# Kernel tuning notes

Measured on AMD Instinct MI355X. Metric: run time of the kernel, lower is better.

## Reference

```python
import jax, jax.numpy as jnp
import numpy as np

B, S, D, N, H = 2, 1024, 1024, 16, 64
R = 2 * S          # max relative length
EPS = 1e-9
INF = 1000000.0
SHIFT = 1          # q_len == context_len branch


def _forward(query, key, value, r, cls_mask, Wq, Wk, bk, Wv, bv, Wo, bo,
             r_w_bias, r_r_bias, r_kernel, r_s_bias, seg_embed, ln_gamma, ln_beta,
             token_type_mat, attention_mask):
    scale = 1.0 / np.sqrt(H).astype(np.float32)
    q = (query @ Wq).reshape(B, S, N, H) * scale          # [b,s,n,h]
    k = (key @ Wk + bk).reshape(B, S, N, H)
    v = (value @ Wv + bv).reshape(B, S, N, H)

    # content score
    content = jnp.einsum('binh,bjnh->bnij', q + r_w_bias * scale, k)

    # relative positional score with shift-gather trick
    r_head = jnp.einsum('td,dnh->tnh', r, r_kernel)        # [2S,n,h]
    pos = jnp.einsum('binh,tnh->bnit', q + r_r_bias * scale, r_head)  # [b,n,s,2S]
    pos = pos.reshape(B, N, R, S)[:, :, SHIFT:, :].reshape(B, N, S, R - SHIFT)[..., :S]
    pos = pos * cls_mask

    # token-type (segment) score: seg_embed[0]=diff, seg_embed[1]=same
    tt_bias = jnp.einsum('binh,snh->bnis', q + r_s_bias * scale, seg_embed)  # [b,n,s,2]
    diff, same = tt_bias[..., :1], tt_bias[..., 1:]
    tt = jnp.where(token_type_mat[:, None], same, diff) * cls_mask           # [b,n,s,s]

    mask = attention_mask.astype(jnp.float32)[:, None, None]                 # [b,1,1,s]
    attn_score = content + pos + tt - INF * (1.0 - mask)
    attn_prob = jax.nn.softmax(attn_score, axis=-1)

    attn_vec = jnp.einsum('bnij,bjnh->binh', attn_prob, v).reshape(B, S, N * H)
    attn_out = attn_vec @ Wo + bo

    x = query + attn_out
    mu = jnp.mean(x, axis=-1, keepdims=True)
    var = jnp.mean(jnp.square(x - mu), axis=-1, keepdims=True)
    return (x - mu) * jax.lax.rsqrt(var + EPS) * ln_gamma + ln_beta


def setup_inputs() -> dict:
    rng = jax.random.key(0)
    ks = jax.random.split(rng, 16)
    init = 0.02
    inp = {
        'query': jax.random.normal(ks[0], (B, S, D), jnp.float32),
        'key':   jax.random.normal(ks[1], (B, S, D), jnp.float32),
        'value': jax.random.normal(ks[2], (B, S, D), jnp.float32),
        'r':     jax.random.normal(ks[3], (R, D), jnp.float32),
        'cls_mask': jnp.ones((S, S), jnp.float32),
        'Wq': jax.random.normal(ks[4], (D, N * H), jnp.float32) * init,
        'Wk': jax.random.normal(ks[5], (D, N * H), jnp.float32) * init,
        'bk': jnp.zeros((N * H,), jnp.float32),
        'Wv': jax.random.normal(ks[6], (D, N * H), jnp.float32) * init,
        'bv': jnp.zeros((N * H,), jnp.float32),
        'Wo': jax.random.normal(ks[7], (N * H, D), jnp.float32) * init,
        'bo': jnp.zeros((D,), jnp.float32),
        'r_w_bias': jax.random.normal(ks[8], (N, H), jnp.float32) * init,
        'r_r_bias': jax.random.normal(ks[9], (N, H), jnp.float32) * init,
        'r_kernel': jax.random.normal(ks[10], (D, N, H), jnp.float32) * init,
        'r_s_bias': jax.random.normal(ks[11], (N, H), jnp.float32) * init,
        'seg_embed': jax.random.normal(ks[12], (2, N, H), jnp.float32) * init,
        'ln_gamma': jnp.ones((D,), jnp.float32),
        'ln_beta': jnp.zeros((D,), jnp.float32),
        'token_type_mat': jax.random.randint(ks[13], (B, S, S), 0, 2).astype(bool),
        'attention_mask': jax.random.randint(ks[14], (B, S), 0, 2).astype(jnp.int32),
    }
    return inp


def reference(query, key, value, r, cls_mask, Wq, Wk, bk, Wv, bv, Wo, bo,
              r_w_bias, r_r_bias, r_kernel, r_s_bias, seg_embed, ln_gamma, ln_beta,
              token_type_mat, attention_mask):
    return _forward(query, key, value, r, cls_mask, Wq, Wk, bk, Wv, bv, Wo, bo,
                    r_w_bias, r_r_bias, r_kernel, r_s_bias, seg_embed, ln_gamma, ln_beta,
                    token_type_mat, attention_mask)
```

## Files before the change

kernel.cpp:

```cpp
#include <hip/hip_runtime.h>

#define S_ 1024

typedef short short8 __attribute__((ext_vector_type(8)));
typedef float floatx4 __attribute__((ext_vector_type(4)));

static __device__ __forceinline__ float b2f(ushort u) {
    union { float f; unsigned int i; } x; x.i = ((unsigned int)u) << 16; return x.f;
}
static __device__ __forceinline__ ushort f2b(float f) {
    union { float f; unsigned int i; } x; x.f = f;
    unsigned int r = (x.i + 0x7fffu + ((x.i >> 16) & 1u)) >> 16;
    return (ushort)r;
}
static __device__ __forceinline__ void async_copy16(ushort* lds, const ushort* g) {
    __builtin_amdgcn_global_load_lds((const __attribute__((address_space(1))) void*)g,
                                     (__attribute__((address_space(3))) void*)lds, 16, 0, 0);
}

struct PreArgs {
    const float* csrc[4]; ushort* cdst[4];
    const float* tsrc[5]; ushort* tdst[5];
    const int* ttm; unsigned long long* ttb;
    const int* am;  unsigned long long* amb;
};
__global__ __launch_bounds__(256) void pre_kernel(PreArgs a) {
    int z = blockIdx.z, tid = threadIdx.x;
    if (z < 4) {
        const float* s = a.csrc[z];
        ushort* d = a.cdst[z];
        size_t idx = ((size_t)blockIdx.x * 256 + tid) * 8;
        float4 f0 = *(const float4*)&s[idx];
        float4 f1 = *(const float4*)&s[idx + 4];
        alignas(16) ushort u[8] = {f2b(f0.x), f2b(f0.y), f2b(f0.z), f2b(f0.w),
                                   f2b(f1.x), f2b(f1.y), f2b(f1.z), f2b(f1.w)};
        *(uint4*)&d[idx] = *(uint4*)u;
    } else if (z < 9) {
        const float* src = a.tsrc[z - 4];
        ushort* dst = a.tdst[z - 4];
        __shared__ float tile[32][33];
        int bx = (blockIdx.x & 31) * 32, by = (blockIdx.x >> 5) * 32;
        int tx = tid & 31, ty = tid >> 5;
#pragma unroll
        for (int i = 0; i < 32; i += 8)
            tile[ty + i][tx] = src[(size_t)(by + ty + i) * 1024 + bx + tx];
        __syncthreads();
#pragma unroll
        for (int i = 0; i < 32; i += 8)
            dst[(size_t)(bx + ty + i) * 1024 + by + tx] = f2b(tile[tx][ty + i]);
    } else {
        int w = tid >> 6, lane = tid & 63;
        int waveid = blockIdx.x * 4 + w;
#pragma unroll
        for (int t = 0; t < 8; t++) {
            int word = waveid * 8 + t;
            unsigned long long m = __ballot(a.ttm[(size_t)word * 64 + lane] != 0);
            if (lane == 0) a.ttb[word] = m;
        }
        if (blockIdx.x == 0 && w == 0) {
            for (int t = 0; t < 32; t++) {
                unsigned long long m = __ballot(a.am[(size_t)t * 64 + lane] != 0);
                if (lane == 0) a.amb[t] = m;
            }
        }
    }
}

struct ProjArgs {
    const ushort* A[4];
    const ushort* BT[4];
    const float* bias[4];
    ushort* C[4];
    float scale[4];
};
__global__ __launch_bounds__(256, 2) void gemm_proj(ProjArgs args) {
    int z = blockIdx.z;
    const ushort* A = args.A[z];
    const ushort* BT = args.BT[z];
    const float* bias = args.bias[z];
    ushort* C = args.C[z];
    float scale = args.scale[z];

    __shared__ alignas(16) ushort As[128 * 64];
    __shared__ alignas(16) ushort Bs[128 * 64];
    int n0 = blockIdx.x * 128, m0 = blockIdx.y * 128;
    int tid = threadIdx.x, lane = tid & 63, w = tid >> 6;
    int wm = (w >> 1) * 64, wn = (w & 1) * 64;
    int li = lane & 15, q4 = lane >> 4;
    int lrow = lane >> 3, lu = (lane & 7) ^ lrow;
    floatx4 acc[4][4] = {};
    for (int k0 = 0; k0 < 1024; k0 += 64) {
        __syncthreads();
#pragma unroll
        for (int t = 0; t < 4; t++) {
            int c = 4 * w + t;
            const ushort* ga = &A[(size_t)(m0 + 8 * c + lrow) * 1024 + k0 + 8 * lu];
            async_copy16(&As[c * 512 + lane * 8], ga);
            const ushort* gb = &BT[(size_t)(n0 + 8 * c + lrow) * 1024 + k0 + 8 * lu];
            async_copy16(&Bs[c * 512 + lane * 8], gb);
        }
        __syncthreads();
        short8 af[2][4], bf[2][4];
#pragma unroll
        for (int kk = 0; kk < 2; kk++) {
#pragma unroll
            for (int ms = 0; ms < 4; ms++)
                af[kk][ms] = *(const short8*)&As[(wm + 16 * ms + li) * 64 +
                                                (((4 * kk + q4) ^ (li & 7)) * 8)];
#pragma unroll
            for (int ns = 0; ns < 4; ns++)
                bf[kk][ns] = *(const short8*)&Bs[(wn + 16 * ns + li) * 64 +
                                                (((4 * kk + q4) ^ (li & 7)) * 8)];
        }
#pragma unroll
        for (int kk = 0; kk < 2; kk++)
#pragma unroll
            for (int ms = 0; ms < 4; ms++)
#pragma unroll
                for (int ns = 0; ns < 4; ns++)
                    acc[ms][ns] = __builtin_amdgcn_mfma_f32_16x16x32_bf16(af[kk][ms], bf[kk][ns],
                                                                          acc[ms][ns], 0, 0, 0);
    }
#pragma unroll
    for (int ns = 0; ns < 4; ns++) {
        int col = n0 + wn + 16 * ns + li;
        float bv = bias ? bias[col] : 0.f;
#pragma unroll
        for (int ms = 0; ms < 4; ms++)
#pragma unroll
            for (int rg = 0; rg < 4; rg++) {
                int row = m0 + wm + 16 * ms + 4 * q4 + rg;
                C[(size_t)row * 1024 + col] = f2b(acc[ms][ns][rg] * scale + bv);
            }
    }
}

__global__ __launch_bounds__(256, 2) void gemm_out(const ushort* __restrict__ A,
                                                   const ushort* __restrict__ BT,
                                                   const float* __restrict__ bias,
                                                   const float* __restrict__ resid,
                                                   float* __restrict__ X) {
    __shared__ alignas(16) ushort As[64 * 64];
    __shared__ alignas(16) ushort Bs[64 * 64];
    int n0 = blockIdx.x * 64, m0 = blockIdx.y * 64;
    int tid = threadIdx.x, lane = tid & 63, w = tid >> 6;
    int wm = (w >> 1) * 32, wn = (w & 1) * 32;
    int li = lane & 15, q4 = lane >> 4;
    int lrow = lane >> 3, lu = (lane & 7) ^ lrow;
    floatx4 acc[2][2] = {};
    for (int k0 = 0; k0 < 1024; k0 += 64) {
        __syncthreads();
#pragma unroll
        for (int t = 0; t < 2; t++) {
            int c = 2 * w + t;
            const ushort* ga = &A[(size_t)(m0 + 8 * c + lrow) * 1024 + k0 + 8 * lu];
            async_copy16(&As[c * 512 + lane * 8], ga);
            const ushort* gb = &BT[(size_t)(n0 + 8 * c + lrow) * 1024 + k0 + 8 * lu];
            async_copy16(&Bs[c * 512 + lane * 8], gb);
        }
        __syncthreads();
        short8 af[2][2], bf[2][2];
#pragma unroll
        for (int kk = 0; kk < 2; kk++) {
#pragma unroll
            for (int ms = 0; ms < 2; ms++)
                af[kk][ms] = *(const short8*)&As[(wm + 16 * ms + li) * 64 +
                                                (((4 * kk + q4) ^ (li & 7)) * 8)];
#pragma unroll
            for (int ns = 0; ns < 2; ns++)
                bf[kk][ns] = *(const short8*)&Bs[(wn + 16 * ns + li) * 64 +
                                                (((4 * kk + q4) ^ (li & 7)) * 8)];
        }
#pragma unroll
        for (int kk = 0; kk < 2; kk++)
#pragma unroll
            for (int ms = 0; ms < 2; ms++)
#pragma unroll
                for (int ns = 0; ns < 2; ns++)
                    acc[ms][ns] = __builtin_amdgcn_mfma_f32_16x16x32_bf16(af[kk][ms], bf[kk][ns],
                                                                          acc[ms][ns], 0, 0, 0);
    }
#pragma unroll
    for (int ns = 0; ns < 2; ns++) {
        int col = n0 + wn + 16 * ns + li;
        float bv = bias[col];
#pragma unroll
        for (int ms = 0; ms < 2; ms++)
#pragma unroll
            for (int rg = 0; rg < 4; rg++) {
                int row = m0 + wm + 16 * ms + 4 * q4 + rg;
                X[(size_t)row * 1024 + col] = acc[ms][ns][rg] + bv + resid[(size_t)row * 1024 + col];
            }
    }
}

__global__ __launch_bounds__(256, 2) void attn_kernel(
    const ushort* __restrict__ qg, const ushort* __restrict__ kg,
    const ushort* __restrict__ vg, const ushort* __restrict__ rh,
    const float* __restrict__ rwb, const float* __restrict__ rrb,
    const float* __restrict__ rsb, const float* __restrict__ seg,
    const unsigned long long* __restrict__ ttb, const unsigned long long* __restrict__ amb,
    ushort* __restrict__ av) {
    __shared__ alignas(16) ushort kt[64][72];
    __shared__ alignas(16) ushort vt[64][72];
    __shared__ alignas(16) ushort rwin[128][72];
    __shared__ alignas(16) ushort pb[4][16][72];
    __shared__ float ttd[64], tts[64];

    int i0 = blockIdx.x * 64, n = blockIdx.y, b = blockIdx.z;
    int tid = threadIdx.x, lane = tid & 63, w = tid >> 6;
    int li = lane & 15, q4 = lane >> 4;
    const float SC = 0.125f;

    {
        int r = tid >> 2, hs = (tid & 3) * 16;
        const ushort* qp = &qg[(size_t)(b * S_ + i0 + r) * 1024 + n * 64 + hs];
        alignas(16) ushort tmp[16];
        *(uint4*)&tmp[0] = *(const uint4*)&qp[0];
        *(uint4*)&tmp[8] = *(const uint4*)&qp[8];
        float d = 0.f, s = 0.f;
#pragma unroll
        for (int e = 0; e < 16; e++) {
            float qv = b2f(tmp[e]);
            int h = n * 64 + hs + e;
            rwin[r][hs + e] = f2b(qv + rwb[h] * SC);
            rwin[64 + r][hs + e] = f2b(qv + rrb[h] * SC);
            float qs = qv + rsb[h] * SC;
            d += qs * seg[h];
            s += qs * seg[1024 + h];
        }
        d += __shfl_xor(d, 1, 64); d += __shfl_xor(d, 2, 64);
        s += __shfl_xor(s, 1, 64); s += __shfl_xor(s, 2, 64);
        if ((tid & 3) == 0) { ttd[r] = d; tts[r] = s; }
    }
    __syncthreads();

    short8 aw0 = *(const short8*)&rwin[16 * w + li][8 * q4];
    short8 aw1 = *(const short8*)&rwin[16 * w + li][32 + 8 * q4];
    short8 ar0 = *(const short8*)&rwin[64 + 16 * w + li][8 * q4];
    short8 ar1 = *(const short8*)&rwin[64 + 16 * w + li][32 + 8 * q4];
    float ttd_l[4], tts_l[4];
#pragma unroll
    for (int r = 0; r < 4; r++) { ttd_l[r] = ttd[16 * w + 4 * q4 + r]; tts_l[r] = tts[16 * w + 4 * q4 + r]; }

    floatx4 o[4] = {};
    float l_i[4] = {0.f, 0.f, 0.f, 0.f};
    const int woff = 48 - 16 * w;

    int kr = tid >> 2, khs = (tid & 3) * 16;
    int g8 = tid >> 5, jp = tid & 31;
    int rr = tid >> 1, rhs2 = (tid & 1) * 32;

    uint4 pk0, pk1, pv0, pv1, pr0, pr1, pr2, pr3;
    unsigned long long ptb[4], pamb;
#define PREFETCH(J0)                                                                       \
    {                                                                                      \
        const ushort* kp = &kg[(size_t)(b * S_ + (J0) + kr) * 1024 + n * 64 + khs];        \
        pk0 = *(const uint4*)kp; pk1 = *(const uint4*)(kp + 8);                            \
        const ushort* vp = &vg[(size_t)(b * S_ + (J0) + 2 * jp) * 1024 + n * 64 + 8 * g8]; \
        pv0 = *(const uint4*)vp; pv1 = *(const uint4*)(vp + 1024);                         \
        int t_ = 1024 + (J0) - i0 - 63 + rr;                                               \
        if (t_ > 2047) t_ = 2047;                                                          \
        const ushort* rp = &rh[(size_t)t_ * 1024 + n * 64 + rhs2];                         \
        pr0 = *(const uint4*)&rp[0];  pr1 = *(const uint4*)&rp[8];                         \
        pr2 = *(const uint4*)&rp[16]; pr3 = *(const uint4*)&rp[24];                        \
        int wj_ = (J0) >> 6;                                                               \
        pamb = amb[b * 16 + wj_];                                                          \
        _Pragma("unroll") for (int r_ = 0; r_ < 4; r_++)                                   \
            ptb[r_] = ttb[((size_t)(b * S_) + i0 + 16 * w + 4 * q4 + r_) * 16 + wj_];      \
    }
    PREFETCH(0);

    for (int j0 = 0; j0 < 1024; j0 += 64) {
        __syncthreads();
        *(uint4*)&kt[kr][khs] = pk0;
        *(uint4*)&kt[kr][khs + 8] = pk1;
        {
            alignas(16) ushort au[8], bu[8];
            *(uint4*)au = pv0; *(uint4*)bu = pv1;
#pragma unroll
            for (int e = 0; e < 8; e++) {
                unsigned int val = (unsigned int)au[e] | ((unsigned int)bu[e] << 16);
                *(unsigned int*)&vt[8 * g8 + e][2 * jp] = val;
            }
        }
        *(uint4*)&rwin[rr][rhs2] = pr0;
        *(uint4*)&rwin[rr][rhs2 + 8] = pr1;
        *(uint4*)&rwin[rr][rhs2 + 16] = pr2;
        *(uint4*)&rwin[rr][rhs2 + 24] = pr3;
        unsigned long long ambw = pamb;
        unsigned long long tb[4] = {ptb[0], ptb[1], ptb[2], ptb[3]};
        __syncthreads();
        if (j0 + 64 < 1024) PREFETCH(j0 + 64);

        floatx4 cs[4] = {};
#pragma unroll
        for (int s = 0; s < 4; s++) {
            short8 b0 = *(const short8*)&kt[16 * s + li][8 * q4];
            short8 b1 = *(const short8*)&kt[16 * s + li][32 + 8 * q4];
            cs[s] = __builtin_amdgcn_mfma_f32_16x16x32_bf16(aw0, b0, cs[s], 0, 0, 0);
            cs[s] = __builtin_amdgcn_mfma_f32_16x16x32_bf16(aw1, b1, cs[s], 0, 0, 0);
        }
        floatx4 pz[5] = {};
#pragma unroll
        for (int s5 = 0; s5 < 5; s5++) {
            short8 b0 = *(const short8*)&rwin[woff + 16 * s5 + li][8 * q4];
            short8 b1 = *(const short8*)&rwin[woff + 16 * s5 + li][32 + 8 * q4];
            pz[s5] = __builtin_amdgcn_mfma_f32_16x16x32_bf16(ar0, b0, pz[s5], 0, 0, 0);
            pz[s5] = __builtin_amdgcn_mfma_f32_16x16x32_bf16(ar1, b1, pz[s5], 0, 0, 0);
        }

        float p[4][4];
#pragma unroll
        for (int r = 0; r < 4; r++) {
            int delta = 15 - 4 * q4 - r;
            float psum = 0.f;
#pragma unroll
            for (int s = 0; s < 4; s++) {
                int c = 16 * s + li + delta;
                int srcl = (lane & 48) | (c & 15);
                float va = __shfl(pz[s][r], srcl, 64);
                float vb = __shfl(pz[s + 1][r], srcl, 64);
                float posv = ((c >> 4) == s) ? va : vb;
                float ttv = ((tb[r] >> (16 * s + li)) & 1) ? tts_l[r] : ttd_l[r];
                float mbv = ((ambw >> (16 * s + li)) & 1) ? 0.f : -1e6f;
                float sc = cs[s][r] + posv + ttv + mbv;
                p[r][s] = __expf(sc);
                psum += p[r][s];
            }
#pragma unroll
            for (int off = 8; off >= 1; off >>= 1) psum += __shfl_xor(psum, off, 64);
            l_i[r] += psum;
        }
#pragma unroll
        for (int r = 0; r < 4; r++)
#pragma unroll
            for (int s = 0; s < 4; s++) pb[w][4 * q4 + r][16 * s + li] = f2b(p[r][s]);
#pragma unroll
        for (int ka = 0; ka < 2; ka++) {
            short8 ap = *(const short8*)&pb[w][li][32 * ka + 8 * q4];
#pragma unroll
            for (int hsub = 0; hsub < 4; hsub++) {
                short8 bv = *(const short8*)&vt[16 * hsub + li][32 * ka + 8 * q4];
                o[hsub] = __builtin_amdgcn_mfma_f32_16x16x32_bf16(ap, bv, o[hsub], 0, 0, 0);
            }
        }
    }
#pragma unroll
    for (int hsub = 0; hsub < 4; hsub++)
#pragma unroll
        for (int r = 0; r < 4; r++) {
            int i = i0 + 16 * w + 4 * q4 + r;
            int h = 16 * hsub + li;
            av[(size_t)(b * S_ + i) * 1024 + n * 64 + h] = f2b(o[hsub][r] / l_i[r]);
        }
#undef PREFETCH
}

__global__ __launch_bounds__(256) void ln_kernel(const float* __restrict__ X,
                                                 const float* __restrict__ gamma,
                                                 const float* __restrict__ beta,
                                                 float* __restrict__ out) {
    int row = blockIdx.x, tid = threadIdx.x;
    float4 v = *(const float4*)&X[(size_t)row * 1024 + tid * 4];
    float sum = v.x + v.y + v.z + v.w;
    float sq = v.x * v.x + v.y * v.y + v.z * v.z + v.w * v.w;
#pragma unroll
    for (int off = 32; off >= 1; off >>= 1) {
        sum += __shfl_xor(sum, off, 64);
        sq += __shfl_xor(sq, off, 64);
    }
    __shared__ float rs[4], rq[4];
    int w = tid >> 6;
    if ((tid & 63) == 0) { rs[w] = sum; rq[w] = sq; }
    __syncthreads();
    sum = rs[0] + rs[1] + rs[2] + rs[3];
    sq = rq[0] + rq[1] + rq[2] + rq[3];
    float mu = sum * (1.f / 1024.f);
    float var = sq * (1.f / 1024.f) - mu * mu;
    float rstd = rsqrtf(fmaxf(var, 0.f) + 1e-9f);
    float4 g = *(const float4*)&gamma[tid * 4];
    float4 be = *(const float4*)&beta[tid * 4];
    float4 o;
    o.x = (v.x - mu) * rstd * g.x + be.x;
    o.y = (v.y - mu) * rstd * g.y + be.y;
    o.z = (v.z - mu) * rstd * g.z + be.z;
    o.w = (v.w - mu) * rstd * g.w + be.w;
    *(float4*)&out[(size_t)row * 1024 + tid * 4] = o;
}

extern "C" void kernel_launch(void* const* d_in, const int* in_sizes, int n_in,
                              void* d_out, int out_size, void* d_ws, size_t ws_size,
                              hipStream_t stream) {
    const float* query = (const float*)d_in[0];
    const float* key   = (const float*)d_in[1];
    const float* value = (const float*)d_in[2];
    const float* r     = (const float*)d_in[3];
    const float* Wq  = (const float*)d_in[5];
    const float* Wk  = (const float*)d_in[6];
    const float* bk  = (const float*)d_in[7];
    const float* Wv  = (const float*)d_in[8];
    const float* bv  = (const float*)d_in[9];
    const float* Wo  = (const float*)d_in[10];
    const float* bo  = (const float*)d_in[11];
    const float* rwb = (const float*)d_in[12];
    const float* rrb = (const float*)d_in[13];
    const float* rk  = (const float*)d_in[14];
    const float* rsb = (const float*)d_in[15];
    const float* seg = (const float*)d_in[16];
    const float* gamma = (const float*)d_in[17];
    const float* beta  = (const float*)d_in[18];
    const int* ttm = (const int*)d_in[19];
    const int* am  = (const int*)d_in[20];
    float* out = (float*)d_out;

    char* ws = (char*)d_ws;
    const size_t MB = (size_t)1 << 20;
    ushort* WqT = (ushort*)(ws + 0 * MB);
    ushort* WkT = (ushort*)(ws + 2 * MB);
    ushort* WvT = (ushort*)(ws + 4 * MB);
    ushort* rkT = (ushort*)(ws + 6 * MB);
    ushort* WoT = (ushort*)(ws + 8 * MB);
    ushort* qf  = (ushort*)(ws + 10 * MB);
    ushort* kf  = (ushort*)(ws + 14 * MB);
    ushort* vf  = (ushort*)(ws + 18 * MB);
    ushort* qb  = (ushort*)(ws + 22 * MB);
    ushort* kb  = (ushort*)(ws + 26 * MB);
    ushort* vb  = (ushort*)(ws + 30 * MB);
    unsigned long long* ttb = (unsigned long long*)(ws + 34 * MB);
    unsigned long long* amb = (unsigned long long*)(ws + 34 * MB + 512 * 1024);
    float*  X   = (float*)(ws + 10 * MB);
    ushort* rf  = (ushort*)d_out;
    ushort* avb = (ushort*)d_out;
    ushort* rhb = (ushort*)((char*)d_out + 4 * MB);

    PreArgs pr;
    pr.csrc[0] = query; pr.csrc[1] = key; pr.csrc[2] = value; pr.csrc[3] = r;
    pr.cdst[0] = qf; pr.cdst[1] = kf; pr.cdst[2] = vf; pr.cdst[3] = rf;
    pr.tsrc[0] = Wq; pr.tsrc[1] = Wk; pr.tsrc[2] = Wv; pr.tsrc[3] = rk; pr.tsrc[4] = Wo;
    pr.tdst[0] = WqT; pr.tdst[1] = WkT; pr.tdst[2] = WvT; pr.tdst[3] = rkT; pr.tdst[4] = WoT;
    pr.ttm = ttm; pr.ttb = ttb; pr.am = am; pr.amb = amb;
    pre_kernel<<<dim3(1024, 1, 10), 256, 0, stream>>>(pr);

    ProjArgs pa;
    pa.A[0] = qf; pa.BT[0] = WqT; pa.bias[0] = nullptr; pa.C[0] = qb;  pa.scale[0] = 0.125f;
    pa.A[1] = kf; pa.BT[1] = WkT; pa.bias[1] = bk;      pa.C[1] = kb;  pa.scale[1] = 1.0f;
    pa.A[2] = vf; pa.BT[2] = WvT; pa.bias[2] = bv;      pa.C[2] = vb;  pa.scale[2] = 1.0f;
    pa.A[3] = rf; pa.BT[3] = rkT; pa.bias[3] = nullptr; pa.C[3] = rhb; pa.scale[3] = 1.0f;
    gemm_proj<<<dim3(8, 16, 4), 256, 0, stream>>>(pa);

    attn_kernel<<<dim3(16, 16, 2), 256, 0, stream>>>(qb, kb, vb, rhb, rwb, rrb, rsb, seg,
                                                     ttb, amb, avb);

    gemm_out<<<dim3(16, 32), 256, 0, stream>>>(avb, WoT, bo, query, X);
    ln_kernel<<<2048, 256, 0, stream>>>(X, gamma, beta, out);
}
```

Before: 241.4 us.

## Load K and relative-position fragments straight to registers, remap blocks, use DPP reductions

The attention kernel no longer stages K and the relative-position window in LDS. Each lane loads its MFMA B-operand fragments directly from global memory into registers and prefetches the next tile after the matching MFMAs. The Q-derived A operands and the token-type dot products are also built in registers, which removes the initial LDS round trip and barrier. The block index is remapped so that XCD-adjacent blocks share (b,n) slices for L2 reuse, the position shift now uses one shuffle instead of two, and the row sums use DPP adds. The cost is more global load instructions with less coalescing and higher register pressure under launch_bounds(256,2).

```diff
diff --git a/kernel.cpp b/kernel.cpp
--- a/kernel.cpp
+++ b/kernel.cpp
@@ -16,6 +16,13 @@
 static __device__ __forceinline__ void async_copy16(ushort* lds, const ushort* g) {
     __builtin_amdgcn_global_load_lds((const __attribute__((address_space(1))) void*)g,
                                      (__attribute__((address_space(3))) void*)lds, 16, 0, 0);
+}
+template <int CTRL>
+static __device__ __forceinline__ float dpp_radd(float x) {
+    union { float f; int i; } a, b;
+    a.f = x;
+    b.i = __builtin_amdgcn_mov_dpp(a.i, CTRL, 0xf, 0xf, true);
+    return x + b.f;
 }
 
 struct PreArgs {
@@ -201,80 +208,99 @@
     const float* __restrict__ rsb, const float* __restrict__ seg,
     const unsigned long long* __restrict__ ttb, const unsigned long long* __restrict__ amb,
     ushort* __restrict__ av) {
-    __shared__ alignas(16) ushort kt[64][72];
     __shared__ alignas(16) ushort vt[64][72];
-    __shared__ alignas(16) ushort rwin[128][72];
     __shared__ alignas(16) ushort pb[4][16][72];
-    __shared__ float ttd[64], tts[64];
-
-    int i0 = blockIdx.x * 64, n = blockIdx.y, b = blockIdx.z;
+
+    int lid = blockIdx.x + 16 * blockIdx.y + 256 * blockIdx.z;
+    int g = lid & 7, tt_ = lid >> 3;
+    int i0 = (tt_ & 15) * 64;
+    int slice = 4 * g + (tt_ >> 4);
+    int n = slice & 15, b = slice >> 4;
+
     int tid = threadIdx.x, lane = tid & 63, w = tid >> 6;
     int li = lane & 15, q4 = lane >> 4;
     const float SC = 0.125f;
-
+    const int kRow = b * S_;
+
+    short8 aw0, aw1, ar0, ar1;
+    float ttd_l[4], tts_l[4];
     {
-        int r = tid >> 2, hs = (tid & 3) * 16;
-        const ushort* qp = &qg[(size_t)(b * S_ + i0 + r) * 1024 + n * 64 + hs];
-        alignas(16) ushort tmp[16];
-        *(uint4*)&tmp[0] = *(const uint4*)&qp[0];
-        *(uint4*)&tmp[8] = *(const uint4*)&qp[8];
+        int qrow = kRow + i0 + 16 * w + li;
+        int h0 = n * 64 + 8 * q4;
+        const ushort* qp = &qg[(size_t)qrow * 1024 + h0];
+        alignas(16) ushort t0[8], t1[8];
+        *(uint4*)t0 = *(const uint4*)qp;
+        *(uint4*)t1 = *(const uint4*)(qp + 32);
+        alignas(16) ushort w0[8], w1[8], r0[8], r1[8];
         float d = 0.f, s = 0.f;
 #pragma unroll
-        for (int e = 0; e < 16; e++) {
-            float qv = b2f(tmp[e]);
-            int h = n * 64 + hs + e;
-            rwin[r][hs + e] = f2b(qv + rwb[h] * SC);
-            rwin[64 + r][hs + e] = f2b(qv + rrb[h] * SC);
-            float qs = qv + rsb[h] * SC;
-            d += qs * seg[h];
-            s += qs * seg[1024 + h];
-        }
-        d += __shfl_xor(d, 1, 64); d += __shfl_xor(d, 2, 64);
-        s += __shfl_xor(s, 1, 64); s += __shfl_xor(s, 2, 64);
-        if ((tid & 3) == 0) { ttd[r] = d; tts[r] = s; }
-    }
-    __syncthreads();
-
-    short8 aw0 = *(const short8*)&rwin[16 * w + li][8 * q4];
-    short8 aw1 = *(const short8*)&rwin[16 * w + li][32 + 8 * q4];
-    short8 ar0 = *(const short8*)&rwin[64 + 16 * w + li][8 * q4];
-    short8 ar1 = *(const short8*)&rwin[64 + 16 * w + li][32 + 8 * q4];
-    float ttd_l[4], tts_l[4];
-#pragma unroll
-    for (int r = 0; r < 4; r++) { ttd_l[r] = ttd[16 * w + 4 * q4 + r]; tts_l[r] = tts[16 * w + 4 * q4 + r]; }
+        for (int e = 0; e < 8; e++) {
+            float qv0 = b2f(t0[e]), qv1 = b2f(t1[e]);
+            int ha = h0 + e, hb = h0 + 32 + e;
+            w0[e] = f2b(qv0 + rwb[ha] * SC);
+            w1[e] = f2b(qv1 + rwb[hb] * SC);
+            r0[e] = f2b(qv0 + rrb[ha] * SC);
+            r1[e] = f2b(qv1 + rrb[hb] * SC);
+            float s0 = qv0 + rsb[ha] * SC, s1 = qv1 + rsb[hb] * SC;
+            d += s0 * seg[ha] + s1 * seg[hb];
+            s += s0 * seg[1024 + ha] + s1 * seg[1024 + hb];
+        }
+        aw0 = *(short8*)w0; aw1 = *(short8*)w1;
+        ar0 = *(short8*)r0; ar1 = *(short8*)r1;
+        d += __shfl_xor(d, 16, 64); d += __shfl_xor(d, 32, 64);
+        s += __shfl_xor(s, 16, 64); s += __shfl_xor(s, 32, 64);
+#pragma unroll
+        for (int r = 0; r < 4; r++) {
+            int srcl = (lane & 48) | (4 * q4 + r);
+            ttd_l[r] = __shfl(d, srcl, 64);
+            tts_l[r] = __shfl(s, srcl, 64);
+        }
+    }
 
     floatx4 o[4] = {};
     float l_i[4] = {0.f, 0.f, 0.f, 0.f};
-    const int woff = 48 - 16 * w;
-
-    int kr = tid >> 2, khs = (tid & 3) * 16;
+
     int g8 = tid >> 5, jp = tid & 31;
-    int rr = tid >> 1, rhs2 = (tid & 1) * 32;
-
-    uint4 pk0, pk1, pv0, pv1, pr0, pr1, pr2, pr3;
+
+    short8 kf0[4], kf1[4], rf0[5], rf1[5];
+    uint4 pv0, pv1;
     unsigned long long ptb[4], pamb;
-#define PREFETCH(J0)                                                                       \
-    {                                                                                      \
-        const ushort* kp = &kg[(size_t)(b * S_ + (J0) + kr) * 1024 + n * 64 + khs];        \
-        pk0 = *(const uint4*)kp; pk1 = *(const uint4*)(kp + 8);                            \
-        const ushort* vp = &vg[(size_t)(b * S_ + (J0) + 2 * jp) * 1024 + n * 64 + 8 * g8]; \
-        pv0 = *(const uint4*)vp; pv1 = *(const uint4*)(vp + 1024);                         \
-        int t_ = 1024 + (J0) - i0 - 63 + rr;                                               \
-        if (t_ > 2047) t_ = 2047;                                                          \
-        const ushort* rp = &rh[(size_t)t_ * 1024 + n * 64 + rhs2];                         \
-        pr0 = *(const uint4*)&rp[0];  pr1 = *(const uint4*)&rp[8];                         \
-        pr2 = *(const uint4*)&rp[16]; pr3 = *(const uint4*)&rp[24];                        \
-        int wj_ = (J0) >> 6;                                                               \
-        pamb = amb[b * 16 + wj_];                                                          \
-        _Pragma("unroll") for (int r_ = 0; r_ < 4; r_++)                                   \
-            ptb[r_] = ttb[((size_t)(b * S_) + i0 + 16 * w + 4 * q4 + r_) * 16 + wj_];      \
-    }
-    PREFETCH(0);
+
+#define LOAD_K(J0)                                                                     \
+    {                                                                                  \
+        _Pragma("unroll") for (int s_ = 0; s_ < 4; s_++) {                             \
+            const ushort* kp =                                                         \
+                &kg[(size_t)(kRow + (J0) + 16 * s_ + li) * 1024 + n * 64 + 8 * q4];    \
+            kf0[s_] = *(const short8*)kp;                                              \
+            kf1[s_] = *(const short8*)(kp + 32);                                       \
+        }                                                                              \
+    }
+#define LOAD_R(J0)                                                                     \
+    {                                                                                  \
+        _Pragma("unroll") for (int s_ = 0; s_ < 5; s_++) {                             \
+            int t_ = 1024 + (J0) - i0 - 15 - 16 * w + 16 * s_ + li;                    \
+            if (t_ > 2047) t_ = 2047;                                                  \
+            const ushort* rp = &rh[(size_t)t_ * 1024 + n * 64 + 8 * q4];               \
+            rf0[s_] = *(const short8*)rp;                                              \
+            rf1[s_] = *(const short8*)(rp + 32);                                       \
+        }                                                                              \
+    }
+#define LOAD_VTB(J0)                                                                   \
+    {                                                                                  \
+        const ushort* vp = &vg[(size_t)(kRow + (J0) + 2 * jp) * 1024 + n * 64 + 8 * g8]; \
+        pv0 = *(const uint4*)vp;                                                       \
+        pv1 = *(const uint4*)(vp + 1024);                                              \
+        int wj_ = (J0) >> 6;                                                           \
+        pamb = amb[b * 16 + wj_];                                                      \
+        _Pragma("unroll") for (int r_ = 0; r_ < 4; r_++)                               \
+            ptb[r_] = ttb[((size_t)kRow + i0 + 16 * w + 4 * q4 + r_) * 16 + wj_];      \
+    }
+    LOAD_K(0);
+    LOAD_R(0);
+    LOAD_VTB(0);
 
     for (int j0 = 0; j0 < 1024; j0 += 64) {
         __syncthreads();
-        *(uint4*)&kt[kr][khs] = pk0;
-        *(uint4*)&kt[kr][khs + 8] = pk1;
         {
             alignas(16) ushort au[8], bu[8];
             *(uint4*)au = pv0; *(uint4*)bu = pv1;
@@ -284,52 +310,48 @@
                 *(unsigned int*)&vt[8 * g8 + e][2 * jp] = val;
             }
         }
-        *(uint4*)&rwin[rr][rhs2] = pr0;
-        *(uint4*)&rwin[rr][rhs2 + 8] = pr1;
-        *(uint4*)&rwin[rr][rhs2 + 16] = pr2;
-        *(uint4*)&rwin[rr][rhs2 + 24] = pr3;
         unsigned long long ambw = pamb;
         unsigned long long tb[4] = {ptb[0], ptb[1], ptb[2], ptb[3]};
         __syncthreads();
-        if (j0 + 64 < 1024) PREFETCH(j0 + 64);
+        bool more = (j0 + 64 < 1024);
+        if (more) LOAD_VTB(j0 + 64);
 
         floatx4 cs[4] = {};
 #pragma unroll
         for (int s = 0; s < 4; s++) {
-            short8 b0 = *(const short8*)&kt[16 * s + li][8 * q4];
-            short8 b1 = *(const short8*)&kt[16 * s + li][32 + 8 * q4];
-            cs[s] = __builtin_amdgcn_mfma_f32_16x16x32_bf16(aw0, b0, cs[s], 0, 0, 0);
-            cs[s] = __builtin_amdgcn_mfma_f32_16x16x32_bf16(aw1, b1, cs[s], 0, 0, 0);
-        }
+            cs[s] = __builtin_amdgcn_mfma_f32_16x16x32_bf16(aw0, kf0[s], cs[s], 0, 0, 0);
+            cs[s] = __builtin_amdgcn_mfma_f32_16x16x32_bf16(aw1, kf1[s], cs[s], 0, 0, 0);
+        }
+        if (more) LOAD_K(j0 + 64);
+
         floatx4 pz[5] = {};
 #pragma unroll
         for (int s5 = 0; s5 < 5; s5++) {
-            short8 b0 = *(const short8*)&rwin[woff + 16 * s5 + li][8 * q4];
-            short8 b1 = *(const short8*)&rwin[woff + 16 * s5 + li][32 + 8 * q4];
-            pz[s5] = __builtin_amdgcn_mfma_f32_16x16x32_bf16(ar0, b0, pz[s5], 0, 0, 0);
-            pz[s5] = __builtin_amdgcn_mfma_f32_16x16x32_bf16(ar1, b1, pz[s5], 0, 0, 0);
-        }
+            pz[s5] = __builtin_amdgcn_mfma_f32_16x16x32_bf16(ar0, rf0[s5], pz[s5], 0, 0, 0);
+            pz[s5] = __builtin_amdgcn_mfma_f32_16x16x32_bf16(ar1, rf1[s5], pz[s5], 0, 0, 0);
+        }
+        if (more) LOAD_R(j0 + 64);
 
         float p[4][4];
 #pragma unroll
         for (int r = 0; r < 4; r++) {
             int delta = 15 - 4 * q4 - r;
+            int srcl = (lane & 48) | ((li + delta) & 15);
             float psum = 0.f;
 #pragma unroll
             for (int s = 0; s < 4; s++) {
-                int c = 16 * s + li + delta;
-                int srcl = (lane & 48) | (c & 15);
-                float va = __shfl(pz[s][r], srcl, 64);
-                float vb = __shfl(pz[s + 1][r], srcl, 64);
-                float posv = ((c >> 4) == s) ? va : vb;
+                float sel = (li < delta) ? pz[s + 1][r] : pz[s][r];
+                float posv = __shfl(sel, srcl, 64);
                 float ttv = ((tb[r] >> (16 * s + li)) & 1) ? tts_l[r] : ttd_l[r];
                 float mbv = ((ambw >> (16 * s + li)) & 1) ? 0.f : -1e6f;
                 float sc = cs[s][r] + posv + ttv + mbv;
                 p[r][s] = __expf(sc);
                 psum += p[r][s];
             }
-#pragma unroll
-            for (int off = 8; off >= 1; off >>= 1) psum += __shfl_xor(psum, off, 64);
+            psum = dpp_radd<0xB1>(psum);
+            psum = dpp_radd<0x4E>(psum);
+            psum = dpp_radd<0x124>(psum);
+            psum = dpp_radd<0x128>(psum);
             l_i[r] += psum;
         }
 #pragma unroll
@@ -352,9 +374,11 @@
         for (int r = 0; r < 4; r++) {
             int i = i0 + 16 * w + 4 * q4 + r;
             int h = 16 * hsub + li;
-            av[(size_t)(b * S_ + i) * 1024 + n * 64 + h] = f2b(o[hsub][r] / l_i[r]);
-        }
-#undef PREFETCH
+            av[(size_t)(kRow + i) * 1024 + n * 64 + h] = f2b(o[hsub][r] / l_i[r]);
+        }
+#undef LOAD_K
+#undef LOAD_R
+#undef LOAD_VTB
 }
 
 __global__ __launch_bounds__(256) void ln_kernel(const float* __restrict__ X,
```

Result: slower. 280.5 us (+16.2%).
